# Kernel optimization log

Measured on AMD Instinct MI355X. Metric: run time of the kernel, lower is better.

## Reference

```python
import jax, jax.numpy as jnp
import numpy as np

T, B, IN, H, OUT, L = 2048, 16, 72, 256, 90, 2


def setup_inputs() -> dict:
    key = jax.random.key(0)
    ks = jax.random.split(key, 12)
    s = 0.05
    x = jax.random.normal(ks[0], (T, B, IN), jnp.float32)
    lengths = jnp.clip(jax.random.randint(ks[1], (B,), 1, T + 1), 1, T)
    W1 = jax.random.normal(ks[2], (H, IN), jnp.float32) * s
    b1 = jax.random.normal(ks[3], (H,), jnp.float32) * s
    Wih = jax.random.normal(ks[4], (L, 4 * H, H), jnp.float32) * s
    Whh = jax.random.normal(ks[5], (L, 4 * H, H), jnp.float32) * s
    bih = jax.random.normal(ks[6], (L, 4 * H), jnp.float32) * s
    bhh = jax.random.normal(ks[7], (L, 4 * H), jnp.float32) * s
    W2 = jax.random.normal(ks[8], (OUT, H), jnp.float32) * s
    b2 = jax.random.normal(ks[9], (OUT,), jnp.float32) * s
    return dict(x=x, lengths=lengths, W1=W1, b1=b1, Wih=Wih, Whh=Whh,
                bih=bih, bhh=bhh, W2=W2, b2=b2)


def _lstm_layer(x, mask, Wih, Whh, bih, bhh):
    # x: [T,B,H], mask: [T,B] bool (True = valid frame)
    Hh = Whh.shape[1]
    Bsz = x.shape[1]
    # input projection for all timesteps at once (the only big GEMM)
    gi = jnp.einsum('tbi,gi->tbg', x, Wih) + bih  # [T,B,4H]

    def step(carry, inp):
        h, c = carry
        g_in, m = inp
        g = g_in + h @ Whh.T + bhh
        i, f, gg, o = jnp.split(g, 4, axis=-1)  # PyTorch gate order i,f,g,o
        c_new = jax.nn.sigmoid(f) * c + jax.nn.sigmoid(i) * jnp.tanh(gg)
        h_new = jax.nn.sigmoid(o) * jnp.tanh(c_new)
        m2 = m[:, None]
        # pack semantics: state frozen past each sequence's length, output zero
        h = jnp.where(m2, h_new, h)
        c = jnp.where(m2, c_new, c)
        return (h, c), jnp.where(m2, h_new, jnp.zeros_like(h_new))

    init = (jnp.zeros((Bsz, Hh), x.dtype), jnp.zeros((Bsz, Hh), x.dtype))
    _, ys = jax.lax.scan(step, init, (gi, mask))
    return ys


def reference(x, lengths, W1, b1, Wih, Whh, bih, bhh, W2, b2):
    # linear1 + relu (dropout=0 -> identity)
    h = jax.nn.relu(jnp.einsum('tbi,hi->tbh', x, W1) + b1)
    mask = jnp.arange(T)[:, None] < lengths[None, :]  # [T,B]
    for l in range(L):
        h = _lstm_layer(h, mask, Wih[l], Whh[l], bih[l], bhh[l])
    y = jnp.einsum('tbh,oh->tbo', h, W2) + b2
    # zero out padded frames (they are discarded by the per-sequence slicing)
    return jnp.where(mask[:, :, None], y, jnp.zeros_like(y))
```

## Files before the change

### kernel.cpp

```cpp
#include <hip/hip_runtime.h>
#include <hip/hip_bf16.h>

#define T_STEPS 2048
#define HID 256
#define INF 72
#define OUTF 90

#define VT 32
#define LT 17
#define HSTR 528

typedef __attribute__((ext_vector_type(4))) float f32x4;
typedef __attribute__((ext_vector_type(8))) short s16x8;
typedef __attribute__((ext_vector_type(4))) short s16x4;

__device__ __forceinline__ unsigned short f2bf(float f) {
  union { float f; unsigned u; } v; v.f = f;
  unsigned r = (v.u + 0x7FFFu + ((v.u >> 16) & 1u)) >> 16;
  return (unsigned short)r;
}
__device__ __forceinline__ float bf2f(unsigned short s) {
  union { unsigned u; float f; } v; v.u = ((unsigned)s) << 16;
  return v.f;
}
__device__ __forceinline__ float sigm(float x) { return 1.f / (1.f + __expf(-x)); }
__device__ __forceinline__ float tanh_f(float x) { return 1.f - 2.f / (1.f + __expf(2.f * x)); }

__global__ __launch_bounds__(256) void inproj(const float* __restrict__ x,
                                              const float* __restrict__ W1,
                                              const float* __restrict__ b1,
                                              float* __restrict__ h0) {
  __shared__ float w1s[HID][INF + 1];
  __shared__ float xs[16][INF];
  const int tid = threadIdx.x;
  const int r0 = blockIdx.x * 16;
  for (int i = tid; i < HID * INF; i += 256) w1s[i / INF][i % INF] = W1[i];
  for (int i = tid; i < 16 * INF; i += 256)
    xs[i / INF][i % INF] = x[(size_t)(r0 + i / INF) * INF + (i % INF)];
  __syncthreads();
  const float bj = b1[tid];
  for (int r = 0; r < 16; ++r) {
    float acc = bj;
#pragma unroll 8
    for (int k = 0; k < INF; ++k) acc += xs[r][k] * w1s[tid][k];
    h0[(size_t)(r0 + r) * HID + tid] = fmaxf(acc, 0.f);
  }
}

__global__ __launch_bounds__(256) void wpack(const float* __restrict__ w,
                                             unsigned short* __restrict__ o) {
  const size_t i = ((size_t)blockIdx.x * 256 + threadIdx.x) * 8;
  f32x4 a = *(const f32x4*)(w + i);
  f32x4 b = *(const f32x4*)(w + i + 4);
  s16x8 v;
#pragma unroll
  for (int e = 0; e < 4; ++e) { v[e] = (short)f2bf(a[e]); v[4 + e] = (short)f2bf(b[e]); }
  *(s16x8*)(o + i) = v;
}

__global__ __launch_bounds__(256) void gi_mfma(const float* __restrict__ h,
                                               const unsigned short* __restrict__ wb,
                                               const float* __restrict__ bih,
                                               const float* __restrict__ bhh,
                                               unsigned short* __restrict__ gi) {
  __shared__ __align__(16) char hs[16 * HSTR];
  __shared__ float bs[1024];
  const int tid = threadIdx.x;
  const int t = blockIdx.x;
  const int lane = tid & 63;
  const int wg = tid >> 6;
  const int j = lane & 15;
  const int hi = lane >> 4;
  for (int i = tid; i < 1024; i += 256) bs[i] = bih[i] + bhh[i];
  {
    const int row = tid >> 4;
    const int c0 = (tid & 15) * 16;
    const float* src = h + ((size_t)t * 16 + row) * 256 + c0;
    f32x4 v0 = *(const f32x4*)(src);
    f32x4 v1 = *(const f32x4*)(src + 4);
    f32x4 v2 = *(const f32x4*)(src + 8);
    f32x4 v3 = *(const f32x4*)(src + 12);
    s16x8 p0, p1;
#pragma unroll
    for (int e = 0; e < 4; ++e) {
      p0[e] = (short)f2bf(v0[e]); p0[4 + e] = (short)f2bf(v1[e]);
      p1[e] = (short)f2bf(v2[e]); p1[4 + e] = (short)f2bf(v3[e]);
    }
    *(s16x8*)(hs + row * HSTR + c0 * 2) = p0;
    *(s16x8*)(hs + row * HSTR + c0 * 2 + 16) = p1;
  }
  __syncthreads();
  const int hread = j * HSTR + hi * 16;
  f32x4 acc[4][4] = {};
#pragma unroll
  for (int kt = 0; kt < 8; ++kt) {
    const int k = kt * 32 + hi * 8;
    const s16x8 a = *(const s16x8*)(hs + hread + kt * 64);
#pragma unroll
    for (int ug2 = 0; ug2 < 4; ++ug2)
#pragma unroll
      for (int q = 0; q < 4; ++q) {
        const s16x8 b = *(const s16x8*)(wb + (((size_t)(q << 8) + wg * 64 + ug2 * 16 + j) << 8) + k);
        acc[ug2][q] = __builtin_amdgcn_mfma_f32_16x16x32_bf16(a, b, acc[ug2][q], 0, 0, 0);
      }
  }
#pragma unroll
  for (int m = 0; m < 2; ++m)
#pragma unroll
    for (int q = 0; q < 4; ++q) {
      const int u0 = wg * 64 + (2 * m) * 16 + j;
      const float b0 = bs[(q << 8) + u0];
      const float b1 = bs[(q << 8) + u0 + 16];
      s16x8 o;
#pragma unroll
      for (int r = 0; r < 4; ++r) {
        o[r]     = (short)f2bf(acc[2 * m][q][r] + b0);
        o[4 + r] = (short)f2bf(acc[2 * m + 1][q][r] + b1);
      }
      *(s16x8*)(gi + ((((size_t)t * 8 + wg * 2 + m) * 4 + q) << 9) + lane * 8) = o;
    }
}


template <int ROLE>
__device__ __forceinline__ void scan_body(
    const unsigned short* __restrict__ gi,
    const unsigned short* __restrict__ whbL,
    const int* __restrict__ lengths,
    unsigned short* __restrict__ hb1,
    float* __restrict__ hout,
    unsigned int* cnt_rel, unsigned int* cntA, unsigned int* cntB,
    char* smem)
{
  const int tid = threadIdx.x;
  const int lane = tid & 63;
  const int w = tid >> 6;
  const int j = lane & 15;
  const int hi = lane >> 4;
  char* wlds = smem;
  char* hbase = smem + 8 * LT * 1024;

  s16x8 bfrV[VT];
#pragma unroll
  for (int ug = 0; ug < 2; ++ug)
#pragma unroll
    for (int kt = 0; kt < 8; ++kt)
#pragma unroll
      for (int q = 0; q < 4; ++q) {
        const int tau = (ug * 8 + kt) * 4 + q;
        if (tau >= VT + LT) continue;
        const int u = w * 32 + ug * 16 + j;
        const s16x8 v = *(const s16x8*)(whbL + ((size_t)(q * 256 + u) << 8) + kt * 32 + hi * 8);
        if (tau < VT) bfrV[tau] = v;
        else *(s16x8*)(wlds + (w * LT + (tau - VT)) * 1024 + lane * 16) = v;
      }
  for (int i = tid; i < 2 * 8448 / 4; i += 512) ((float*)hbase)[i] = 0.f;
  __syncthreads();

  int len[4];
#pragma unroll
  for (int r = 0; r < 4; ++r) len[r] = lengths[hi * 4 + r];
  float c[8] = {};
  unsigned short hprev[8] = {};

  const unsigned short* gwp = whbL + (size_t)(w * 32 + 16 + j) * 256 + hi * 8;
  const int hread = j * HSTR + hi * 16;
  unsigned cred = 0;

#define GKT(i) (4 + ((i) + 1) / 4)
#define GQ(i)  (((i) + 1) & 3)

  for (int tg = 0; tg < T_STEPS; tg += 4) {
    if (ROLE == 1) {
      while (cred < (unsigned)(tg + 4)) {
        unsigned a = __hip_atomic_load(cntA, __ATOMIC_ACQUIRE, __HIP_MEMORY_SCOPE_AGENT);
        unsigned b = __hip_atomic_load(cntB, __ATOMIC_ACQUIRE, __HIP_MEMORY_SCOPE_AGENT);
        cred = a < b ? a : b;
        if (cred < (unsigned)(tg + 4)) __builtin_amdgcn_s_sleep(2);
      }
    }
    for (int ts = 0; ts < 4; ++ts) {
      const int t = tg + ts;
      const char* hc = hbase + (t & 1) * 8448;
      char* hn = hbase + ((t + 1) & 1) * 8448;
      const unsigned short* gb = gi + (((size_t)t * 8 + w) * 4) * 512 + lane * 8;

      s16x4 gv0[4], gv1[4];
#pragma unroll
      for (int q = 0; q < 4; ++q) gv0[q] = *(const s16x4*)(gb + q * 512);
      s16x8 gw[15];
#pragma unroll
      for (int i = 0; i < 5; ++i) gw[i] = *(const s16x8*)(gwp + GQ(i) * 65536 + GKT(i) * 32);

      f32x4 acc[4] = {};
#pragma unroll
      for (int kt = 0; kt < 8; ++kt) {
        const s16x8 a = *(const s16x8*)(hc + hread + kt * 64);
#pragma unroll
        for (int q = 0; q < 4; ++q)
          acc[q] = __builtin_amdgcn_mfma_f32_16x16x32_bf16(a, bfrV[kt * 4 + q], acc[q], 0, 0, 0);
      }
      {
        const int u = w * 32 + j;
#pragma unroll
        for (int r = 0; r < 4; ++r) {
          const float g0 = acc[0][r] + bf2f((unsigned short)gv0[0][r]);
          const float g1 = acc[1][r] + bf2f((unsigned short)gv0[1][r]);
          const float g2 = acc[2][r] + bf2f((unsigned short)gv0[2][r]);
          const float g3 = acc[3][r] + bf2f((unsigned short)gv0[3][r]);
          const float i_ = sigm(g0), f_ = sigm(g1), tg_ = tanh_f(g2), o_ = sigm(g3);
          const float cn = f_ * c[r] + i_ * tg_;
          const float hv = o_ * tanh_f(cn);
          const bool m = t < len[r];
          c[r] = m ? cn : c[r];
          const unsigned short hb = m ? f2bf(hv) : hprev[r];
          hprev[r] = hb;
          const int b = hi * 4 + r;
          *(unsigned short*)(hn + b * HSTR + u * 2) = hb;
          if (ROLE == 0) hb1[(size_t)t * 4096 + b * 256 + u] = m ? hb : (unsigned short)0;
          else           hout[((size_t)t * 16 + b) * 256 + u] = m ? hv : 0.f;
        }
      }
#pragma unroll
      for (int q = 0; q < 4; ++q) gv1[q] = *(const s16x4*)(gb + q * 512 + 4);
#pragma unroll
      for (int i = 5; i < 10; ++i) gw[i] = *(const s16x8*)(gwp + GQ(i) * 65536 + GKT(i) * 32);

#pragma unroll
      for (int q = 0; q < 4; ++q) { f32x4 z = {}; acc[q] = z; }
#pragma unroll
      for (int kt = 0; kt < 8; ++kt) {
        const s16x8 a = *(const s16x8*)(hc + hread + kt * 64);
#pragma unroll
        for (int q = 0; q < 4; ++q) {
          const int tau = (8 + kt) * 4 + q;
          s16x8 bw;
          if (tau < VT) bw = bfrV[tau];
          else if (tau < VT + LT) bw = *(const s16x8*)(wlds + (w * LT + (tau - VT)) * 1024 + lane * 16);
          else bw = gw[(kt - 4) * 4 + q - 1];
          acc[q] = __builtin_amdgcn_mfma_f32_16x16x32_bf16(a, bw, acc[q], 0, 0, 0);
        }
        if (kt == 1) {
#pragma unroll
          for (int i = 10; i < 15; ++i) gw[i] = *(const s16x8*)(gwp + GQ(i) * 65536 + GKT(i) * 32);
        }
      }
      {
        const int u = w * 32 + 16 + j;
#pragma unroll
        for (int r = 0; r < 4; ++r) {
          const int ci = 4 + r;
          const float g0 = acc[0][r] + bf2f((unsigned short)gv1[0][r]);
          const float g1 = acc[1][r] + bf2f((unsigned short)gv1[1][r]);
          const float g2 = acc[2][r] + bf2f((unsigned short)gv1[2][r]);
          const float g3 = acc[3][r] + bf2f((unsigned short)gv1[3][r]);
          const float i_ = sigm(g0), f_ = sigm(g1), tg_ = tanh_f(g2), o_ = sigm(g3);
          const float cn = f_ * c[ci] + i_ * tg_;
          const float hv = o_ * tanh_f(cn);
          const bool m = t < len[r];
          c[ci] = m ? cn : c[ci];
          const unsigned short hb = m ? f2bf(hv) : hprev[ci];
          hprev[ci] = hb;
          const int b = hi * 4 + r;
          *(unsigned short*)(hn + b * HSTR + u * 2) = hb;
          if (ROLE == 0) hb1[(size_t)t * 4096 + b * 256 + u] = m ? hb : (unsigned short)0;
          else           hout[((size_t)t * 16 + b) * 256 + u] = m ? hv : 0.f;
        }
      }
      if (ts == 3) {
        asm volatile("s_waitcnt vmcnt(0) lgkmcnt(0)" ::: "memory");
        __builtin_amdgcn_s_barrier();
        if (ROLE == 0 && tid == 0)
          __hip_atomic_store(cnt_rel, (unsigned)(t + 1), __ATOMIC_RELEASE, __HIP_MEMORY_SCOPE_AGENT);
      } else {
        asm volatile("s_waitcnt lgkmcnt(0)" ::: "memory");
        __builtin_amdgcn_s_barrier();
      }
      asm volatile("" ::: "memory");
    }
  }
#undef GKT
#undef GQ
}

__device__ __forceinline__ void gi2_body(int qbase,
    const unsigned short* __restrict__ hb1,
    const unsigned short* __restrict__ wb2,
    const float* __restrict__ bih2, const float* __restrict__ bhh2,
    unsigned short* __restrict__ gf2,
    unsigned int* cnt_src, unsigned int* cnt_out)
{
  const int tid = threadIdx.x;
  const int lane = tid & 63;
  const int w = tid >> 6;
  const int j = lane & 15;
  const int hi = lane >> 4;

  s16x8 wfr[2][2][8];
  float bsum[2][2];
#pragma unroll
  for (int qh = 0; qh < 2; ++qh)
#pragma unroll
    for (int ug = 0; ug < 2; ++ug) {
      const int col = (qbase + qh) * 256 + w * 32 + ug * 16 + j;
      bsum[qh][ug] = bih2[col] + bhh2[col];
#pragma unroll
      for (int kt = 0; kt < 8; ++kt)
        wfr[qh][ug][kt] = *(const s16x8*)(wb2 + ((size_t)col << 8) + kt * 32 + hi * 8);
    }

  unsigned cred = 0;
  for (int tg = 0; tg < T_STEPS; tg += 4) {
    while (cred < (unsigned)(tg + 4)) {
      cred = __hip_atomic_load(cnt_src, __ATOMIC_ACQUIRE, __HIP_MEMORY_SCOPE_AGENT);
      if (cred < (unsigned)(tg + 4)) __builtin_amdgcn_s_sleep(2);
    }
    for (int ts = 0; ts < 4; ++ts) {
      const int t = tg + ts;
      const unsigned short* ab = hb1 + (size_t)t * 4096 + j * 256 + hi * 8;
      f32x4 acc[2][2] = {};
#pragma unroll
      for (int kt = 0; kt < 8; ++kt) {
        const s16x8 a = *(const s16x8*)(ab + kt * 32);
#pragma unroll
        for (int qh = 0; qh < 2; ++qh)
#pragma unroll
          for (int ug = 0; ug < 2; ++ug)
            acc[qh][ug] = __builtin_amdgcn_mfma_f32_16x16x32_bf16(a, wfr[qh][ug][kt], acc[qh][ug], 0, 0, 0);
      }
#pragma unroll
      for (int qh = 0; qh < 2; ++qh) {
        s16x8 o;
#pragma unroll
        for (int r = 0; r < 4; ++r) {
          o[r]     = (short)f2bf(acc[qh][0][r] + bsum[qh][0]);
          o[4 + r] = (short)f2bf(acc[qh][1][r] + bsum[qh][1]);
        }
        *(s16x8*)(gf2 + ((((size_t)t * 8 + w) * 4 + qbase + qh) << 9) + lane * 8) = o;
      }
    }
    asm volatile("s_waitcnt vmcnt(0)" ::: "memory");
    __builtin_amdgcn_s_barrier();
    if (tid == 0)
      __hip_atomic_store(cnt_out, (unsigned)(tg + 4), __ATOMIC_RELEASE, __HIP_MEMORY_SCOPE_AGENT);
    asm volatile("" ::: "memory");
  }
}

__global__ __launch_bounds__(512, 2) void fused_pipe(
    const unsigned short* __restrict__ gf1,
    const unsigned short* __restrict__ whb,
    const unsigned short* __restrict__ wb,
    const float* __restrict__ bih, const float* __restrict__ bhh,
    const int* __restrict__ lengths,
    unsigned short* hb1, unsigned short* gf2, float* hout2,
    unsigned int* cnts)
{
  extern __shared__ char smem[];
  const int bid = blockIdx.x;
  if (bid == 0)
    scan_body<0>(gf1, whb, lengths, hb1, nullptr, cnts, nullptr, nullptr, smem);
  else if (bid == 1)
    gi2_body(0, hb1, wb + 262144, bih + 1024, bhh + 1024, gf2, cnts, cnts + 16);
  else if (bid == 2)
    gi2_body(2, hb1, wb + 262144, bih + 1024, bhh + 1024, gf2, cnts, cnts + 32);
  else
    scan_body<1>(gf2, whb + 262144, lengths, nullptr, hout2, nullptr, cnts + 16, cnts + 32, smem);
}

__global__ __launch_bounds__(256) void outproj(const float* __restrict__ h2,
                                               const float* __restrict__ W2,
                                               const float* __restrict__ b2,
                                               const int* __restrict__ lengths,
                                               float* __restrict__ y) {
  __shared__ float w2s[OUTF][HID + 1];
  __shared__ float hs[8][HID + 1];
  const int tid = threadIdx.x;
  const int r0 = blockIdx.x * 8;
  for (int i = tid; i < OUTF * HID; i += 256) w2s[i / HID][i % HID] = W2[i];
  for (int i = tid; i < 8 * HID; i += 256)
    hs[i / HID][i % HID] = h2[(size_t)(r0 + i / HID) * HID + (i % HID)];
  __syncthreads();
  for (int oi = tid; oi < 8 * OUTF; oi += 256) {
    const int r = oi / OUTF, o = oi % OUTF;
    const int row = r0 + r, t = row >> 4, b = row & 15;
    float acc = b2[o];
#pragma unroll 8
    for (int k = 0; k < HID; ++k) acc += hs[r][k] * w2s[o][k];
    y[(size_t)row * OUTF + o] = (t < lengths[b]) ? acc : 0.f;
  }
}

extern "C" void kernel_launch(void* const* d_in, const int* in_sizes, int n_in,
                              void* d_out, int out_size, void* d_ws, size_t ws_size,
                              hipStream_t stream) {
  const float* x      = (const float*)d_in[0];
  const int*   lengths= (const int*)d_in[1];
  const float* W1     = (const float*)d_in[2];
  const float* b1     = (const float*)d_in[3];
  const float* Wih    = (const float*)d_in[4];
  const float* Whh    = (const float*)d_in[5];
  const float* bih    = (const float*)d_in[6];
  const float* bhh    = (const float*)d_in[7];
  const float* W2     = (const float*)d_in[8];
  const float* b2     = (const float*)d_in[9];
  float* out = (float*)d_out;

  char* ws = (char*)d_ws;
  float*          h0   = (float*)(ws);
  unsigned short* gf1  = (unsigned short*)(ws + 33554432);
  unsigned short* hb1  = (unsigned short*)(ws + 100663296);
  unsigned short* gf2  = (unsigned short*)(ws + 117440512);
  float*          h2o  = (float*)(ws + 184549376);
  unsigned short* wb   = (unsigned short*)(ws + 218103808);
  unsigned short* whb  = (unsigned short*)(ws + 219152384);
  unsigned int*   cnts = (unsigned int*)(ws + 220200960);

  hipFuncSetAttribute((const void*)fused_pipe,
                      hipFuncAttributeMaxDynamicSharedMemorySize, 156160);

  wpack<<<256, 256, 0, stream>>>(Wih, wb);
  wpack<<<256, 256, 0, stream>>>(Whh, whb);
  inproj<<<2048, 256, 0, stream>>>(x, W1, b1, h0);
  gi_mfma<<<2048, 256, 0, stream>>>(h0, wb, bih, bhh, gf1);

  hipMemsetAsync((void*)cnts, 0, 256, stream);
  fused_pipe<<<4, 512, 156160, stream>>>(gf1, whb, wb, bih, bhh, lengths,
                                         hb1, gf2, h2o, cnts);

  outproj<<<4096, 256, 0, stream>>>(h2o, W2, b2, lengths, out);
}
```

Baseline: 11.26 ms.

## Widen recurrent scan blocks to 16 waves with all Whh fragments in registers

Measured after the change: 25.29 ms. 2.25x slower.

```diff
diff --git a/kernel.cpp b/kernel.cpp
--- a/kernel.cpp
+++ b/kernel.cpp
@@ -5,14 +5,11 @@
 #define HID 256
 #define INF 72
 #define OUTF 90
-
-#define VT 32
-#define LT 17
 #define HSTR 528
+#define HBUF (16 * HSTR)
 
 typedef __attribute__((ext_vector_type(4))) float f32x4;
 typedef __attribute__((ext_vector_type(8))) short s16x8;
-typedef __attribute__((ext_vector_type(4))) short s16x4;
 
 __device__ __forceinline__ unsigned short f2bf(float f) {
   union { float f; unsigned u; } v; v.f = f;
@@ -23,8 +20,12 @@
   union { unsigned u; float f; } v; v.u = ((unsigned)s) << 16;
   return v.f;
 }
-__device__ __forceinline__ float sigm(float x) { return 1.f / (1.f + __expf(-x)); }
-__device__ __forceinline__ float tanh_f(float x) { return 1.f - 2.f / (1.f + __expf(2.f * x)); }
+__device__ __forceinline__ float sigm(float x) {
+  return __builtin_amdgcn_rcpf(1.f + __builtin_amdgcn_exp2f(-1.44269504f * x));
+}
+__device__ __forceinline__ float tanh_f(float x) {
+  return 1.f - 2.f * __builtin_amdgcn_rcpf(1.f + __builtin_amdgcn_exp2f(2.88539008f * x));
+}
 
 __global__ __launch_bounds__(256) void inproj(const float* __restrict__ x,
                                               const float* __restrict__ W1,
@@ -105,20 +106,21 @@
       }
   }
 #pragma unroll
-  for (int m = 0; m < 2; ++m)
-#pragma unroll
-    for (int q = 0; q < 4; ++q) {
-      const int u0 = wg * 64 + (2 * m) * 16 + j;
-      const float b0 = bs[(q << 8) + u0];
-      const float b1 = bs[(q << 8) + u0 + 16];
-      s16x8 o;
-#pragma unroll
-      for (int r = 0; r < 4; ++r) {
-        o[r]     = (short)f2bf(acc[2 * m][q][r] + b0);
-        o[4 + r] = (short)f2bf(acc[2 * m + 1][q][r] + b1);
-      }
-      *(s16x8*)(gi + ((((size_t)t * 8 + wg * 2 + m) * 4 + q) << 9) + lane * 8) = o;
-    }
+  for (int ug2 = 0; ug2 < 4; ++ug2) {
+    const int sw = wg * 4 + ug2;
+    const int u0 = wg * 64 + ug2 * 16 + j;
+    s16x8 o0, o1;
+#pragma unroll
+    for (int r = 0; r < 4; ++r) {
+      o0[r]     = (short)f2bf(acc[ug2][0][r] + bs[u0]);
+      o0[4 + r] = (short)f2bf(acc[ug2][1][r] + bs[256 + u0]);
+      o1[r]     = (short)f2bf(acc[ug2][2][r] + bs[512 + u0]);
+      o1[4 + r] = (short)f2bf(acc[ug2][3][r] + bs[768 + u0]);
+    }
+    unsigned short* dst = gi + ((size_t)(t * 16 + sw) * 64 + lane) * 16;
+    *(s16x8*)(dst) = o0;
+    *(s16x8*)(dst + 8) = o1;
+  }
 }
 
 
@@ -129,143 +131,98 @@
     const int* __restrict__ lengths,
     unsigned short* __restrict__ hb1,
     float* __restrict__ hout,
-    unsigned int* cnt_rel, unsigned int* cntA, unsigned int* cntB,
+    unsigned int* cnt_rel, unsigned int* cnt_src,
     char* smem)
 {
-  const int tid = threadIdx.x;
+  const int tid  = threadIdx.x;
   const int lane = tid & 63;
-  const int w = tid >> 6;
-  const int j = lane & 15;
-  const int hi = lane >> 4;
-  char* wlds = smem;
-  char* hbase = smem + 8 * LT * 1024;
-
-  s16x8 bfrV[VT];
-#pragma unroll
-  for (int ug = 0; ug < 2; ++ug)
-#pragma unroll
-    for (int kt = 0; kt < 8; ++kt)
-#pragma unroll
-      for (int q = 0; q < 4; ++q) {
-        const int tau = (ug * 8 + kt) * 4 + q;
-        if (tau >= VT + LT) continue;
-        const int u = w * 32 + ug * 16 + j;
-        const s16x8 v = *(const s16x8*)(whbL + ((size_t)(q * 256 + u) << 8) + kt * 32 + hi * 8);
-        if (tau < VT) bfrV[tau] = v;
-        else *(s16x8*)(wlds + (w * LT + (tau - VT)) * 1024 + lane * 16) = v;
-      }
-  for (int i = tid; i < 2 * 8448 / 4; i += 512) ((float*)hbase)[i] = 0.f;
+  const int w    = tid >> 6;
+  const int j    = lane & 15;
+  const int hi   = lane >> 4;
+  const int u    = w * 16 + j;
+
+  s16x8 wfr[32];
+#pragma unroll
+  for (int kt = 0; kt < 8; ++kt)
+#pragma unroll
+    for (int q = 0; q < 4; ++q)
+      wfr[kt * 4 + q] =
+          *(const s16x8*)(whbL + ((size_t)(q * 256 + u) << 8) + kt * 32 + hi * 8);
+
+  for (int i = tid; i < 2 * HBUF / 4; i += 1024) ((float*)smem)[i] = 0.f;
+
+  int len[4];
+#pragma unroll
+  for (int r = 0; r < 4; ++r) len[r] = lengths[hi * 4 + r];
+  float c[4] = {};
+  unsigned short hprev[4] = {};
+
+  const unsigned short* gp = gi + ((size_t)w * 64 + lane) * 16;
   __syncthreads();
 
-  int len[4];
-#pragma unroll
-  for (int r = 0; r < 4; ++r) len[r] = lengths[hi * 4 + r];
-  float c[8] = {};
-  unsigned short hprev[8] = {};
-
-  const unsigned short* gwp = whbL + (size_t)(w * 32 + 16 + j) * 256 + hi * 8;
+  unsigned cred = 0;
+  if (ROLE == 1) {
+    const unsigned t0 = (8 <= T_STEPS) ? 8u : (unsigned)T_STEPS;
+    while (cred < t0) {
+      cred = __hip_atomic_load(cnt_src, __ATOMIC_ACQUIRE, __HIP_MEMORY_SCOPE_AGENT);
+      if (cred < t0) __builtin_amdgcn_s_sleep(2);
+    }
+  }
+
+  s16x8 g0 = *(const s16x8*)(gp);
+  s16x8 g1 = *(const s16x8*)(gp + 8);
   const int hread = j * HSTR + hi * 16;
-  unsigned cred = 0;
-
-#define GKT(i) (4 + ((i) + 1) / 4)
-#define GQ(i)  (((i) + 1) & 3)
 
   for (int tg = 0; tg < T_STEPS; tg += 4) {
     if (ROLE == 1) {
-      while (cred < (unsigned)(tg + 4)) {
-        unsigned a = __hip_atomic_load(cntA, __ATOMIC_ACQUIRE, __HIP_MEMORY_SCOPE_AGENT);
-        unsigned b = __hip_atomic_load(cntB, __ATOMIC_ACQUIRE, __HIP_MEMORY_SCOPE_AGENT);
-        cred = a < b ? a : b;
-        if (cred < (unsigned)(tg + 4)) __builtin_amdgcn_s_sleep(2);
-      }
-    }
+      const unsigned target = (tg + 8 <= T_STEPS) ? (unsigned)(tg + 8) : (unsigned)T_STEPS;
+      while (cred < target) {
+        cred = __hip_atomic_load(cnt_src, __ATOMIC_ACQUIRE, __HIP_MEMORY_SCOPE_AGENT);
+        if (cred < target) __builtin_amdgcn_s_sleep(2);
+      }
+    }
+#pragma unroll
     for (int ts = 0; ts < 4; ++ts) {
       const int t = tg + ts;
-      const char* hc = hbase + (t & 1) * 8448;
-      char* hn = hbase + ((t + 1) & 1) * 8448;
-      const unsigned short* gb = gi + (((size_t)t * 8 + w) * 4) * 512 + lane * 8;
-
-      s16x4 gv0[4], gv1[4];
-#pragma unroll
-      for (int q = 0; q < 4; ++q) gv0[q] = *(const s16x4*)(gb + q * 512);
-      s16x8 gw[15];
-#pragma unroll
-      for (int i = 0; i < 5; ++i) gw[i] = *(const s16x8*)(gwp + GQ(i) * 65536 + GKT(i) * 32);
-
-      f32x4 acc[4] = {};
+      const char* hc = smem + (t & 1) * HBUF;
+      char* hn = smem + ((t + 1) & 1) * HBUF;
+      f32x4 acc[4];
+#pragma unroll
+      for (int r = 0; r < 4; ++r) {
+        acc[0][r] = bf2f((unsigned short)g0[r]);
+        acc[1][r] = bf2f((unsigned short)g0[4 + r]);
+        acc[2][r] = bf2f((unsigned short)g1[r]);
+        acc[3][r] = bf2f((unsigned short)g1[4 + r]);
+      }
+      {
+        const int tn = (t + 1 < T_STEPS) ? t + 1 : t;
+        const unsigned short* gn = gp + (size_t)tn * 16384;
+        g0 = *(const s16x8*)(gn);
+        g1 = *(const s16x8*)(gn + 8);
+      }
 #pragma unroll
       for (int kt = 0; kt < 8; ++kt) {
         const s16x8 a = *(const s16x8*)(hc + hread + kt * 64);
 #pragma unroll
         for (int q = 0; q < 4; ++q)
-          acc[q] = __builtin_amdgcn_mfma_f32_16x16x32_bf16(a, bfrV[kt * 4 + q], acc[q], 0, 0, 0);
-      }
-      {
-        const int u = w * 32 + j;
-#pragma unroll
-        for (int r = 0; r < 4; ++r) {
-          const float g0 = acc[0][r] + bf2f((unsigned short)gv0[0][r]);
-          const float g1 = acc[1][r] + bf2f((unsigned short)gv0[1][r]);
-          const float g2 = acc[2][r] + bf2f((unsigned short)gv0[2][r]);
-          const float g3 = acc[3][r] + bf2f((unsigned short)gv0[3][r]);
-          const float i_ = sigm(g0), f_ = sigm(g1), tg_ = tanh_f(g2), o_ = sigm(g3);
-          const float cn = f_ * c[r] + i_ * tg_;
-          const float hv = o_ * tanh_f(cn);
-          const bool m = t < len[r];
-          c[r] = m ? cn : c[r];
-          const unsigned short hb = m ? f2bf(hv) : hprev[r];
-          hprev[r] = hb;
-          const int b = hi * 4 + r;
-          *(unsigned short*)(hn + b * HSTR + u * 2) = hb;
-          if (ROLE == 0) hb1[(size_t)t * 4096 + b * 256 + u] = m ? hb : (unsigned short)0;
-          else           hout[((size_t)t * 16 + b) * 256 + u] = m ? hv : 0.f;
-        }
-      }
-#pragma unroll
-      for (int q = 0; q < 4; ++q) gv1[q] = *(const s16x4*)(gb + q * 512 + 4);
-#pragma unroll
-      for (int i = 5; i < 10; ++i) gw[i] = *(const s16x8*)(gwp + GQ(i) * 65536 + GKT(i) * 32);
-
-#pragma unroll
-      for (int q = 0; q < 4; ++q) { f32x4 z = {}; acc[q] = z; }
-#pragma unroll
-      for (int kt = 0; kt < 8; ++kt) {
-        const s16x8 a = *(const s16x8*)(hc + hread + kt * 64);
-#pragma unroll
-        for (int q = 0; q < 4; ++q) {
-          const int tau = (8 + kt) * 4 + q;
-          s16x8 bw;
-          if (tau < VT) bw = bfrV[tau];
-          else if (tau < VT + LT) bw = *(const s16x8*)(wlds + (w * LT + (tau - VT)) * 1024 + lane * 16);
-          else bw = gw[(kt - 4) * 4 + q - 1];
-          acc[q] = __builtin_amdgcn_mfma_f32_16x16x32_bf16(a, bw, acc[q], 0, 0, 0);
-        }
-        if (kt == 1) {
-#pragma unroll
-          for (int i = 10; i < 15; ++i) gw[i] = *(const s16x8*)(gwp + GQ(i) * 65536 + GKT(i) * 32);
-        }
-      }
-      {
-        const int u = w * 32 + 16 + j;
-#pragma unroll
-        for (int r = 0; r < 4; ++r) {
-          const int ci = 4 + r;
-          const float g0 = acc[0][r] + bf2f((unsigned short)gv1[0][r]);
-          const float g1 = acc[1][r] + bf2f((unsigned short)gv1[1][r]);
-          const float g2 = acc[2][r] + bf2f((unsigned short)gv1[2][r]);
-          const float g3 = acc[3][r] + bf2f((unsigned short)gv1[3][r]);
-          const float i_ = sigm(g0), f_ = sigm(g1), tg_ = tanh_f(g2), o_ = sigm(g3);
-          const float cn = f_ * c[ci] + i_ * tg_;
-          const float hv = o_ * tanh_f(cn);
-          const bool m = t < len[r];
-          c[ci] = m ? cn : c[ci];
-          const unsigned short hb = m ? f2bf(hv) : hprev[ci];
-          hprev[ci] = hb;
-          const int b = hi * 4 + r;
-          *(unsigned short*)(hn + b * HSTR + u * 2) = hb;
-          if (ROLE == 0) hb1[(size_t)t * 4096 + b * 256 + u] = m ? hb : (unsigned short)0;
-          else           hout[((size_t)t * 16 + b) * 256 + u] = m ? hv : 0.f;
-        }
+          acc[q] = __builtin_amdgcn_mfma_f32_16x16x32_bf16(a, wfr[kt * 4 + q], acc[q], 0, 0, 0);
+      }
+#pragma unroll
+      for (int r = 0; r < 4; ++r) {
+        const float i_  = sigm(acc[0][r]);
+        const float f_  = sigm(acc[1][r]);
+        const float tg_ = tanh_f(acc[2][r]);
+        const float o_  = sigm(acc[3][r]);
+        const float cn = f_ * c[r] + i_ * tg_;
+        const float hv = o_ * tanh_f(cn);
+        const bool m = t < len[r];
+        c[r] = m ? cn : c[r];
+        const unsigned short hb = m ? f2bf(hv) : hprev[r];
+        hprev[r] = hb;
+        const int b = hi * 4 + r;
+        *(unsigned short*)(hn + b * HSTR + u * 2) = hb;
+        if (ROLE == 0) hb1[(size_t)t * 4096 + b * 256 + u] = m ? hb : (unsigned short)0;
+        else           hout[((size_t)t * 16 + b) * 256 + u] = m ? hv : 0.f;
       }
       if (ts == 3) {
         asm volatile("s_waitcnt vmcnt(0) lgkmcnt(0)" ::: "memory");
@@ -279,11 +236,9 @@
       asm volatile("" ::: "memory");
     }
   }
-#undef GKT
-#undef GQ
-}
-
-__device__ __forceinline__ void gi2_body(int qbase,
+}
+
+__device__ __forceinline__ void gi2_body(
     const unsigned short* __restrict__ hb1,
     const unsigned short* __restrict__ wb2,
     const float* __restrict__ bih2, const float* __restrict__ bhh2,
@@ -295,19 +250,18 @@
   const int w = tid >> 6;
   const int j = lane & 15;
   const int hi = lane >> 4;
-
-  s16x8 wfr[2][2][8];
-  float bsum[2][2];
-#pragma unroll
-  for (int qh = 0; qh < 2; ++qh)
-#pragma unroll
-    for (int ug = 0; ug < 2; ++ug) {
-      const int col = (qbase + qh) * 256 + w * 32 + ug * 16 + j;
-      bsum[qh][ug] = bih2[col] + bhh2[col];
-#pragma unroll
-      for (int kt = 0; kt < 8; ++kt)
-        wfr[qh][ug][kt] = *(const s16x8*)(wb2 + ((size_t)col << 8) + kt * 32 + hi * 8);
-    }
+  const int u = w * 16 + j;
+
+  s16x8 wfr[32];
+  float bsum[4];
+#pragma unroll
+  for (int q = 0; q < 4; ++q) {
+    const int col = q * 256 + u;
+    bsum[q] = bih2[col] + bhh2[col];
+#pragma unroll
+    for (int kt = 0; kt < 8; ++kt)
+      wfr[kt * 4 + q] = *(const s16x8*)(wb2 + ((size_t)col << 8) + kt * 32 + hi * 8);
+  }
 
   unsigned cred = 0;
   for (int tg = 0; tg < T_STEPS; tg += 4) {
@@ -315,29 +269,33 @@
       cred = __hip_atomic_load(cnt_src, __ATOMIC_ACQUIRE, __HIP_MEMORY_SCOPE_AGENT);
       if (cred < (unsigned)(tg + 4)) __builtin_amdgcn_s_sleep(2);
     }
+#pragma unroll
     for (int ts = 0; ts < 4; ++ts) {
       const int t = tg + ts;
       const unsigned short* ab = hb1 + (size_t)t * 4096 + j * 256 + hi * 8;
-      f32x4 acc[2][2] = {};
+      f32x4 acc[4];
+#pragma unroll
+      for (int q = 0; q < 4; ++q)
+#pragma unroll
+        for (int r = 0; r < 4; ++r) acc[q][r] = bsum[q];
 #pragma unroll
       for (int kt = 0; kt < 8; ++kt) {
         const s16x8 a = *(const s16x8*)(ab + kt * 32);
 #pragma unroll
-        for (int qh = 0; qh < 2; ++qh)
-#pragma unroll
-          for (int ug = 0; ug < 2; ++ug)
-            acc[qh][ug] = __builtin_amdgcn_mfma_f32_16x16x32_bf16(a, wfr[qh][ug][kt], acc[qh][ug], 0, 0, 0);
-      }
-#pragma unroll
-      for (int qh = 0; qh < 2; ++qh) {
-        s16x8 o;
-#pragma unroll
-        for (int r = 0; r < 4; ++r) {
-          o[r]     = (short)f2bf(acc[qh][0][r] + bsum[qh][0]);
-          o[4 + r] = (short)f2bf(acc[qh][1][r] + bsum[qh][1]);
-        }
-        *(s16x8*)(gf2 + ((((size_t)t * 8 + w) * 4 + qbase + qh) << 9) + lane * 8) = o;
-      }
+        for (int q = 0; q < 4; ++q)
+          acc[q] = __builtin_amdgcn_mfma_f32_16x16x32_bf16(a, wfr[kt * 4 + q], acc[q], 0, 0, 0);
+      }
+      s16x8 o0, o1;
+#pragma unroll
+      for (int r = 0; r < 4; ++r) {
+        o0[r]     = (short)f2bf(acc[0][r]);
+        o0[4 + r] = (short)f2bf(acc[1][r]);
+        o1[r]     = (short)f2bf(acc[2][r]);
+        o1[4 + r] = (short)f2bf(acc[3][r]);
+      }
+      unsigned short* dst = gf2 + ((size_t)(t * 16 + w) * 64 + lane) * 16;
+      *(s16x8*)(dst) = o0;
+      *(s16x8*)(dst + 8) = o1;
     }
     asm volatile("s_waitcnt vmcnt(0)" ::: "memory");
     __builtin_amdgcn_s_barrier();
@@ -347,7 +305,7 @@
   }
 }
 
-__global__ __launch_bounds__(512, 2) void fused_pipe(
+__global__ __launch_bounds__(1024, 1) void fused_pipe(
     const unsigned short* __restrict__ gf1,
     const unsigned short* __restrict__ whb,
     const unsigned short* __restrict__ wb,
@@ -357,15 +315,12 @@
     unsigned int* cnts)
 {
   extern __shared__ char smem[];
-  const int bid = blockIdx.x;
-  if (bid == 0)
-    scan_body<0>(gf1, whb, lengths, hb1, nullptr, cnts, nullptr, nullptr, smem);
-  else if (bid == 1)
-    gi2_body(0, hb1, wb + 262144, bih + 1024, bhh + 1024, gf2, cnts, cnts + 16);
-  else if (bid == 2)
-    gi2_body(2, hb1, wb + 262144, bih + 1024, bhh + 1024, gf2, cnts, cnts + 32);
+  if (blockIdx.x == 0)
+    scan_body<0>(gf1, whb, lengths, hb1, nullptr, cnts, nullptr, smem);
+  else if (blockIdx.x == 1)
+    gi2_body(hb1, wb + 262144, bih + 1024, bhh + 1024, gf2, cnts, cnts + 16);
   else
-    scan_body<1>(gf2, whb + 262144, lengths, nullptr, hout2, nullptr, cnts + 16, cnts + 32, smem);
+    scan_body<1>(gf2, whb + 262144, lengths, nullptr, hout2, nullptr, cnts + 16, smem);
 }
 
 __global__ __launch_bounds__(256) void outproj(const float* __restrict__ h2,
@@ -416,17 +371,14 @@
   unsigned short* whb  = (unsigned short*)(ws + 219152384);
   unsigned int*   cnts = (unsigned int*)(ws + 220200960);
 
-  hipFuncSetAttribute((const void*)fused_pipe,
-                      hipFuncAttributeMaxDynamicSharedMemorySize, 156160);
-
   wpack<<<256, 256, 0, stream>>>(Wih, wb);
   wpack<<<256, 256, 0, stream>>>(Whh, whb);
   inproj<<<2048, 256, 0, stream>>>(x, W1, b1, h0);
   gi_mfma<<<2048, 256, 0, stream>>>(h0, wb, bih, bhh, gf1);
 
   hipMemsetAsync((void*)cnts, 0, 256, stream);
-  fused_pipe<<<4, 512, 156160, stream>>>(gf1, whb, wb, bih, bhh, lengths,
-                                         hb1, gf2, h2o, cnts);
+  fused_pipe<<<3, 1024, 2 * HBUF, stream>>>(gf1, whb, wb, bih, bhh, lengths,
+                                            hb1, gf2, h2o, cnts);
 
   outproj<<<4096, 256, 0, stream>>>(h2o, W2, b2, lengths, out);
 }
```
